# Kernel optimization log

Hardware: AMD Instinct MI355X
Metric: run time of the kernel (lower is better)

Reference implementation:

```python
import jax, jax.numpy as jnp
import numpy as np
from jax import lax


def setup_inputs() -> dict:
    key = jax.random.key(0)
    ks = jax.random.split(key, 14)
    B, T, I, H = 64, 512, 1024, 1024
    s = 0.02  # small init so gates stay in a sane range
    inp = {"x": jax.random.normal(ks[0], (B, T, I), jnp.float32)}
    names = ["wii", "whi", "bi", "wif", "whf", "bf", "wig", "whg", "bg", "wio", "who", "bo"]
    shapes = [(I, H), (H, H), (H,)] * 4
    for n, sh, k in zip(names, shapes, ks[1:]):
        inp[n] = jax.random.normal(k, sh, jnp.float32) * s
    return inp


def reference(x, wii, whi, bi, wif, whf, bf, wig, whg, bg, wio, who, bo):
    B, T, _ = x.shape
    H = bi.shape[0]
    # Pack the 4 gates (i, f, g, o) into single GEMMs.
    Wx = jnp.concatenate([wii, wif, wig, wio], axis=1)  # [I, 4H]
    Wh = jnp.concatenate([whi, whf, whg, who], axis=1)  # [H, 4H]
    b = jnp.concatenate([bi, bf, bg, bo])               # [4H]
    # Precompute all input projections in one big GEMM: [B, T, 4H]
    xproj = jnp.einsum("bti,ig->btg", x, Wx) + b

    def step(carry, xt):
        ht, ct = carry  # [B, H] each
        gates = xt + ht @ Wh  # [B, 4H]
        i = jax.nn.sigmoid(gates[:, 0 * H:1 * H])
        f = jax.nn.sigmoid(gates[:, 1 * H:2 * H])
        g = jnp.tanh(gates[:, 2 * H:3 * H])
        o = jax.nn.sigmoid(gates[:, 3 * H:4 * H])
        ct = f * ct + i * g
        ht = o * jnp.tanh(ct)
        return (ht, ct), ht

    h0 = jnp.zeros((B, H), x.dtype)
    c0 = jnp.zeros((B, H), x.dtype)
    (ht, ct), hseq = lax.scan(step, (h0, c0), xproj.transpose(1, 0, 2))
    hseq = hseq.transpose(1, 0, 2)  # [B, T, H]
    return hseq, ht, ct
```

## Files before the change

### kernel.cpp

```cpp
#include <hip/hip_runtime.h>
#include <cstddef>
#include <cstdint>


typedef __bf16 bf16_t;
typedef __bf16 bf16x8 __attribute__((ext_vector_type(8)));
typedef __bf16 bf16x4 __attribute__((ext_vector_type(4)));
typedef float  f32x4  __attribute__((ext_vector_type(4)));

#define MFMA16(a, b, c) __builtin_amdgcn_mfma_f32_16x16x32_bf16((a), (b), (c), 0, 0, 0)

#define BB   64
#define TT   512
#define HH   1024
#define G4H  4096

#define XPROJ_OFF  0ull
#define WX_OFF     268435456ull
#define WH_OFF     (WX_OFF + 8388608ull)
#define BC_OFF     (WH_OFF + 8388608ull)
#define HB_OFF     (BC_OFF + 16384ull)
#define BAR_OFF    (HB_OFF + 262144ull)

__device__ __forceinline__ float fsig(float x) {
    return 1.0f / (1.0f + __expf(-x));
}
__device__ __forceinline__ float ftanh(float x) {
    return 1.0f - 2.0f / (__expf(2.0f * x) + 1.0f);
}

__global__ void transpose_pack(const float* __restrict__ s0, const float* __restrict__ s1,
                               const float* __restrict__ s2, const float* __restrict__ s3,
                               const float* __restrict__ s4, const float* __restrict__ s5,
                               const float* __restrict__ s6, const float* __restrict__ s7,
                               bf16_t* __restrict__ wxt, bf16_t* __restrict__ wht) {
    __shared__ float tile[64][65];
    const int z = blockIdx.z;
    const float* src = (z == 0) ? s0 : (z == 1) ? s1 : (z == 2) ? s2 : (z == 3) ? s3
                      : (z == 4) ? s4 : (z == 5) ? s5 : (z == 6) ? s6 : s7;
    bf16_t* dst = ((z < 4) ? wxt : wht) + (size_t)(z & 3) * 1024 * 1024;
    const int k0 = blockIdx.x * 64, h0 = blockIdx.y * 64;
    const int t = threadIdx.x;
#pragma unroll
    for (int i = 0; i < 16; ++i) {
        int kk = (t >> 6) * 16 + i, hh = t & 63;
        tile[kk][hh] = src[(size_t)(k0 + kk) * 1024 + h0 + hh];
    }
    __syncthreads();
#pragma unroll
    for (int i = 0; i < 16; ++i) {
        int hh = (t >> 6) * 16 + i, kk = t & 63;
        dst[(size_t)(h0 + hh) * 1024 + k0 + kk] = (bf16_t)tile[kk][hh];
    }
}

__global__ void pack_bias(const float* __restrict__ bi, const float* __restrict__ bf_,
                          const float* __restrict__ bg, const float* __restrict__ bo,
                          float* __restrict__ bc) {
    int n = blockIdx.x * 256 + threadIdx.x;
    int g = n >> 10, h = n & 1023;
    const float* s = (g == 0) ? bi : (g == 1) ? bf_ : (g == 2) ? bg : bo;
    bc[n] = s[h];
}

__global__ __launch_bounds__(256, 2) void gemm_xproj(
    const float* __restrict__ x, const bf16_t* __restrict__ wx,
    const float* __restrict__ bc, bf16_t* __restrict__ xp) {
    __shared__ bf16_t Als[128][72];
    __shared__ bf16_t Bls[128][72];
    const int tid = threadIdx.x;
    const int n0 = blockIdx.x * 128, m0 = blockIdx.y * 128;
    const int lane = tid & 63, w = tid >> 6;
    const int wm = w >> 1, wn = w & 1;
    const int col = lane & 15, quad = lane >> 4;
    const int rowA = tid >> 4, ksegA = (tid & 15) * 4;
    const int rowB = tid >> 3, chunkB = tid & 7;
    f32x4 acc[4][4] = {};

    for (int kt = 0; kt < 16; ++kt) {
        const int k0 = kt * 64;
        __syncthreads();
#pragma unroll
        for (int i = 0; i < 8; ++i) {
            int r = rowA + i * 16;
            float4 v = *(const float4*)&x[(size_t)(m0 + r) * 1024 + k0 + ksegA];
            bf16x4 pv = { (bf16_t)v.x, (bf16_t)v.y, (bf16_t)v.z, (bf16_t)v.w };
            *(bf16x4*)&Als[r][ksegA] = pv;
        }
#pragma unroll
        for (int i = 0; i < 4; ++i) {
            int r = rowB + i * 32;
            *(bf16x8*)&Bls[r][chunkB * 8] =
                *(const bf16x8*)&wx[(size_t)(n0 + r) * 1024 + k0 + chunkB * 8];
        }
        __syncthreads();
#pragma unroll
        for (int kq = 0; kq < 64; kq += 32) {
            bf16x8 a[4], b[4];
#pragma unroll
            for (int s = 0; s < 4; ++s) {
                a[s] = *(const bf16x8*)&Als[wm * 64 + s * 16 + col][kq + quad * 8];
                b[s] = *(const bf16x8*)&Bls[wn * 64 + s * 16 + col][kq + quad * 8];
            }
#pragma unroll
            for (int sm = 0; sm < 4; ++sm)
#pragma unroll
                for (int sn = 0; sn < 4; ++sn)
                    acc[sm][sn] = MFMA16(a[sm], b[sn], acc[sm][sn]);
        }
    }
#pragma unroll
    for (int sm = 0; sm < 4; ++sm) {
        int mbase = m0 + wm * 64 + sm * 16 + quad * 4;
#pragma unroll
        for (int sn = 0; sn < 4; ++sn) {
            int n = n0 + wn * 64 + sn * 16 + col;
            float bias = bc[n];
#pragma unroll
            for (int reg = 0; reg < 4; ++reg) {
                int mm = mbase + reg;
                int b = mm >> 9, t = mm & 511;
                xp[(size_t)((t << 6) + b) * 4096 + n] = (bf16_t)(acc[sm][sn][reg] + bias);
            }
        }
    }
}

__global__ __launch_bounds__(256, 1) void lstm_rec(
    const bf16_t* __restrict__ xproj, const bf16_t* __restrict__ whc,
    bf16_t* __restrict__ hbuf, float* __restrict__ out,
    unsigned int* __restrict__ bar) {
    __shared__ bf16_t wh[16][1032];
    __shared__ float  gl[64][17];
    __shared__ __align__(8) unsigned short gl2[64][4];
    const int tid = threadIdx.x;
    const int bid = blockIdx.x;
    unsigned int* goflag = bar + 384;

    {
        int r = tid >> 4, sub = tid & 15;
        int n = (r >> 2) * 1024 + bid * 4 + (r & 3);
        const bf16_t* src = whc + (size_t)n * 1024;
#pragma unroll
        for (int j = 0; j < 8; ++j) {
            int e = (j * 16 + sub) * 8;
            *(bf16x8*)&wh[r][e] = *(const bf16x8*)&src[e];
        }
    }
    __syncthreads();

    const int w = tid >> 6, lane = tid & 63;
    const int col = lane & 15, quad = lane >> 4;
    const int rowA = w * 16 + col;
    const int bb0  = w * 16 + quad * 4;
    const int b2 = tid >> 2, cc = tid & 3;
    const int hcol = bid * 4 + cc;
    const int ng = (col >> 2) * 1024 + bid * 4 + (col & 3);

    float cstate = 0.0f;
    float* hseq = out;
    float* hT = out + (size_t)BB * TT * HH;
    float* cT = hT + BB * HH;

    float xpre[4];
#pragma unroll
    for (int reg = 0; reg < 4; ++reg)
        xpre[reg] = (float)xproj[(size_t)(bb0 + reg) * 4096 + ng];

    for (int t = 0; t < TT; ++t) {
        const bf16_t* hprev = hbuf + (size_t)(t & 1) * (BB * HH);
        bf16_t* hnext = hbuf + (size_t)((t + 1) & 1) * (BB * HH);

        const bf16_t* hbase = hprev + (size_t)rowA * 1024 + quad * 8;
        bf16x8 af[32];
#define LDH(i, o) asm volatile("global_load_dwordx4 %0, %1, off offset:" o " sc0 sc1" \
                               : "=v"(af[i]) : "v"(hbase))
        LDH(0, "0");     LDH(1, "64");    LDH(2, "128");   LDH(3, "192");
        LDH(4, "256");   LDH(5, "320");   LDH(6, "384");   LDH(7, "448");
        LDH(8, "512");   LDH(9, "576");   LDH(10, "640");  LDH(11, "704");
        LDH(12, "768");  LDH(13, "832");  LDH(14, "896");  LDH(15, "960");
        LDH(16, "1024"); LDH(17, "1088"); LDH(18, "1152"); LDH(19, "1216");
        LDH(20, "1280"); LDH(21, "1344"); LDH(22, "1408"); LDH(23, "1472");
        LDH(24, "1536"); LDH(25, "1600"); LDH(26, "1664"); LDH(27, "1728");
        LDH(28, "1792"); LDH(29, "1856"); LDH(30, "1920"); LDH(31, "1984");
#undef LDH
        asm volatile("s_waitcnt vmcnt(0)" ::: "memory");
        __builtin_amdgcn_sched_barrier(0);

        f32x4 acc = {0.f, 0.f, 0.f, 0.f};
#pragma unroll
        for (int kq = 0; kq < 32; ++kq) {
            bf16x8 bfr = *(const bf16x8*)&wh[col][kq * 32 + quad * 8];
            acc = MFMA16(af[kq], bfr, acc);
        }

#pragma unroll
        for (int reg = 0; reg < 4; ++reg) {
            int bb = bb0 + reg;
            gl[bb][col] = acc[reg] + xpre[reg];
        }

        float iv = fsig(gl[b2][cc]);
        float fv = fsig(gl[b2][4 + cc]);
        float gv = ftanh(gl[b2][8 + cc]);
        float ov = fsig(gl[b2][12 + cc]);
        cstate = fv * cstate + iv * gv;
        float hv = ov * ftanh(cstate);

        __builtin_nontemporal_store(hv, &hseq[(size_t)b2 * (TT * HH) + t * HH + hcol]);
        bf16_t hvb = (bf16_t)hv;
        gl2[b2][cc] = *(const unsigned short*)&hvb;

        if (t == TT - 1) {
            __builtin_nontemporal_store(hv, &hT[b2 * HH + hcol]);
            __builtin_nontemporal_store(cstate, &cT[b2 * HH + hcol]);
            break;
        }

        __syncthreads();

        const unsigned tgt = (unsigned)(t + 1);
        const size_t xoff = (size_t)((t + 1) * 64 + bb0) * 4096 + ng;
        if (w == 0) {
            unsigned long long pk = *(const unsigned long long*)&gl2[lane][0];
            __hip_atomic_store((unsigned long long*)(hnext + (size_t)lane * HH + bid * 4),
                               pk, __ATOMIC_RELAXED, __HIP_MEMORY_SCOPE_AGENT);
            asm volatile("s_waitcnt vmcnt(0)" ::: "memory");
            if (lane == 0)
                __hip_atomic_store(&bar[bid], tgt, __ATOMIC_RELAXED,
                                   __HIP_MEMORY_SCOPE_AGENT);
            asm volatile("" ::: "memory");
#pragma unroll
            for (int reg = 0; reg < 4; ++reg)
                xpre[reg] = (float)xproj[xoff + (size_t)reg * 4096];

            if (bid == 0) {
                unsigned int* sl = bar + lane * 4;
                for (;;) {
                    unsigned v0 = __hip_atomic_load(sl + 0, __ATOMIC_RELAXED,
                                                    __HIP_MEMORY_SCOPE_AGENT);
                    unsigned v1 = __hip_atomic_load(sl + 1, __ATOMIC_RELAXED,
                                                    __HIP_MEMORY_SCOPE_AGENT);
                    unsigned v2 = __hip_atomic_load(sl + 2, __ATOMIC_RELAXED,
                                                    __HIP_MEMORY_SCOPE_AGENT);
                    unsigned v3 = __hip_atomic_load(sl + 3, __ATOMIC_RELAXED,
                                                    __HIP_MEMORY_SCOPE_AGENT);
                    int ok = (v0 >= tgt) & (v1 >= tgt) & (v2 >= tgt) & (v3 >= tgt);
                    if (__all(ok)) break;
                    __builtin_amdgcn_s_sleep(2);
                }
                if (lane == 0)
                    __hip_atomic_store(goflag, tgt, __ATOMIC_RELAXED,
                                       __HIP_MEMORY_SCOPE_AGENT);
            } else {
                for (;;) {
                    unsigned g = __hip_atomic_load(goflag, __ATOMIC_RELAXED,
                                                   __HIP_MEMORY_SCOPE_AGENT);
                    if (g >= tgt) break;
                    __builtin_amdgcn_s_sleep(2);
                }
            }
        } else {
#pragma unroll
            for (int reg = 0; reg < 4; ++reg)
                xpre[reg] = (float)xproj[xoff + (size_t)reg * 4096];
        }
        __syncthreads();
    }
}

extern "C" void kernel_launch(void* const* d_in, const int* in_sizes, int n_in,
                              void* d_out, int out_size, void* d_ws, size_t ws_size,
                              hipStream_t stream) {
    (void)in_sizes; (void)n_in; (void)out_size; (void)ws_size;
    const float* x   = (const float*)d_in[0];
    const float* wii = (const float*)d_in[1];
    const float* whi = (const float*)d_in[2];
    const float* bi  = (const float*)d_in[3];
    const float* wif = (const float*)d_in[4];
    const float* whf = (const float*)d_in[5];
    const float* bfb = (const float*)d_in[6];
    const float* wig = (const float*)d_in[7];
    const float* whg = (const float*)d_in[8];
    const float* bg  = (const float*)d_in[9];
    const float* wio = (const float*)d_in[10];
    const float* who = (const float*)d_in[11];
    const float* bo  = (const float*)d_in[12];

    char* ws = (char*)d_ws;
    bf16_t*   xp   = (bf16_t*)(ws + XPROJ_OFF);
    bf16_t*   wxt  = (bf16_t*)(ws + WX_OFF);
    bf16_t*   wht  = (bf16_t*)(ws + WH_OFF);
    float*    bc   = (float*)(ws + BC_OFF);
    bf16_t*   hbuf = (bf16_t*)(ws + HB_OFF);
    unsigned* bar  = (unsigned*)(ws + BAR_OFF);

    hipMemsetAsync(hbuf, 0, 262144 + 4096, stream);

    transpose_pack<<<dim3(16, 16, 8), 256, 0, stream>>>(wii, wif, wig, wio,
                                                        whi, whf, whg, who, wxt, wht);
    pack_bias<<<16, 256, 0, stream>>>(bi, bfb, bg, bo, bc);
    gemm_xproj<<<dim3(32, 256), 256, 0, stream>>>(x, wxt, bc, xp);
    lstm_rec<<<256, 256, 0, stream>>>(xp, wht, hbuf, (float*)d_out, bar);
}
```

Baseline: 4.723 ms.

## Halve recurrent grid to 128 blocks with 8 hidden columns each and flat barrier

Each persistent block of the recurrent kernel now owns 8 hidden units (32 gate rows) instead of 4, so the grid drops from 256 to 128 blocks, each issuing two MFMA chains over the same loaded h fragment. The two-level barrier (block 0 gathers, then broadcasts a go flag) becomes a flat barrier where every block polls all 128 flags directly. Each thread now handles two adjacent units with packed bf16 xproj loads and writes h to the global buffer itself. The aim is to halve redundant h reads, cut the barrier's serial hop and shrink per-step latency, at the cost of more per-block MFMA work and more polling traffic.

```diff
diff --git a/kernel.cpp b/kernel.cpp
--- a/kernel.cpp
+++ b/kernel.cpp
@@ -6,7 +6,9 @@
 typedef __bf16 bf16_t;
 typedef __bf16 bf16x8 __attribute__((ext_vector_type(8)));
 typedef __bf16 bf16x4 __attribute__((ext_vector_type(4)));
+typedef __bf16 bf16x2 __attribute__((ext_vector_type(2)));
 typedef float  f32x4  __attribute__((ext_vector_type(4)));
+typedef float  f32x2  __attribute__((ext_vector_type(2)));
 
 #define MFMA16(a, b, c) __builtin_amdgcn_mfma_f32_16x16x32_bf16((a), (b), (c), 0, 0, 0)
 
@@ -14,6 +16,7 @@
 #define TT   512
 #define HH   1024
 #define G4H  4096
+#define NBLK 128
 
 #define XPROJ_OFF  0ull
 #define WX_OFF     268435456ull
@@ -130,20 +133,17 @@
     const bf16_t* __restrict__ xproj, const bf16_t* __restrict__ whc,
     bf16_t* __restrict__ hbuf, float* __restrict__ out,
     unsigned int* __restrict__ bar) {
-    __shared__ bf16_t wh[16][1032];
-    __shared__ float  gl[64][17];
-    __shared__ __align__(8) unsigned short gl2[64][4];
+    __shared__ bf16_t wh[32][1032];
+    __shared__ float  gl[64][36];
     const int tid = threadIdx.x;
     const int bid = blockIdx.x;
-    unsigned int* goflag = bar + 384;
 
     {
-        int r = tid >> 4, sub = tid & 15;
-        int n = (r >> 2) * 1024 + bid * 4 + (r & 3);
-        const bf16_t* src = whc + (size_t)n * 1024;
-#pragma unroll
-        for (int j = 0; j < 8; ++j) {
-            int e = (j * 16 + sub) * 8;
+        int r = tid >> 3, seg = tid & 7;
+        const bf16_t* src = whc + (size_t)((r >> 3) * 1024 + bid * 8 + (r & 7)) * 1024;
+#pragma unroll
+        for (int j = 0; j < 16; ++j) {
+            int e = seg * 128 + j * 8;
             *(bf16x8*)&wh[r][e] = *(const bf16x8*)&src[e];
         }
     }
@@ -153,19 +153,19 @@
     const int col = lane & 15, quad = lane >> 4;
     const int rowA = w * 16 + col;
     const int bb0  = w * 16 + quad * 4;
-    const int b2 = tid >> 2, cc = tid & 3;
-    const int hcol = bid * 4 + cc;
-    const int ng = (col >> 2) * 1024 + bid * 4 + (col & 3);
-
-    float cstate = 0.0f;
+    const int b2 = tid >> 2;
+    const int c2 = (tid & 3) * 2;
+    const int hcol = bid * 8 + c2;
+
+    float cs0 = 0.0f, cs1 = 0.0f;
     float* hseq = out;
     float* hT = out + (size_t)BB * TT * HH;
     float* cT = hT + BB * HH;
 
-    float xpre[4];
-#pragma unroll
-    for (int reg = 0; reg < 4; ++reg)
-        xpre[reg] = (float)xproj[(size_t)(bb0 + reg) * 4096 + ng];
+    unsigned xq[4];
+#pragma unroll
+    for (int g = 0; g < 4; ++g)
+        xq[g] = *(const unsigned*)&xproj[(size_t)b2 * 4096 + g * 1024 + hcol];
 
     for (int t = 0; t < TT; ++t) {
         const bf16_t* hprev = hbuf + (size_t)(t & 1) * (BB * HH);
@@ -187,83 +187,75 @@
         asm volatile("s_waitcnt vmcnt(0)" ::: "memory");
         __builtin_amdgcn_sched_barrier(0);
 
-        f32x4 acc = {0.f, 0.f, 0.f, 0.f};
+        f32x4 acc0 = {0.f, 0.f, 0.f, 0.f};
+        f32x4 acc1 = {0.f, 0.f, 0.f, 0.f};
 #pragma unroll
         for (int kq = 0; kq < 32; ++kq) {
-            bf16x8 bfr = *(const bf16x8*)&wh[col][kq * 32 + quad * 8];
-            acc = MFMA16(af[kq], bfr, acc);
+            bf16x8 b0 = *(const bf16x8*)&wh[col][kq * 32 + quad * 8];
+            bf16x8 b1 = *(const bf16x8*)&wh[16 + col][kq * 32 + quad * 8];
+            acc0 = MFMA16(af[kq], b0, acc0);
+            acc1 = MFMA16(af[kq], b1, acc1);
         }
 
 #pragma unroll
         for (int reg = 0; reg < 4; ++reg) {
-            int bb = bb0 + reg;
-            gl[bb][col] = acc[reg] + xpre[reg];
-        }
-
-        float iv = fsig(gl[b2][cc]);
-        float fv = fsig(gl[b2][4 + cc]);
-        float gv = ftanh(gl[b2][8 + cc]);
-        float ov = fsig(gl[b2][12 + cc]);
-        cstate = fv * cstate + iv * gv;
-        float hv = ov * ftanh(cstate);
-
-        __builtin_nontemporal_store(hv, &hseq[(size_t)b2 * (TT * HH) + t * HH + hcol]);
-        bf16_t hvb = (bf16_t)hv;
-        gl2[b2][cc] = *(const unsigned short*)&hvb;
+            gl[bb0 + reg][col]      = acc0[reg];
+            gl[bb0 + reg][16 + col] = acc1[reg];
+        }
+
+        float a0l = gl[b2][0 * 8 + c2]     + __uint_as_float(xq[0] << 16);
+        float a0h = gl[b2][0 * 8 + c2 + 1] + __uint_as_float(xq[0] & 0xffff0000u);
+        float a1l = gl[b2][1 * 8 + c2]     + __uint_as_float(xq[1] << 16);
+        float a1h = gl[b2][1 * 8 + c2 + 1] + __uint_as_float(xq[1] & 0xffff0000u);
+        float a2l = gl[b2][2 * 8 + c2]     + __uint_as_float(xq[2] << 16);
+        float a2h = gl[b2][2 * 8 + c2 + 1] + __uint_as_float(xq[2] & 0xffff0000u);
+        float a3l = gl[b2][3 * 8 + c2]     + __uint_as_float(xq[3] << 16);
+        float a3h = gl[b2][3 * 8 + c2 + 1] + __uint_as_float(xq[3] & 0xffff0000u);
+        cs0 = fsig(a1l) * cs0 + fsig(a0l) * ftanh(a2l);
+        cs1 = fsig(a1h) * cs1 + fsig(a0h) * ftanh(a2h);
+        float hv0 = fsig(a3l) * ftanh(cs0);
+        float hv1 = fsig(a3h) * ftanh(cs1);
+
+        f32x2 hv2 = { hv0, hv1 };
+        __builtin_nontemporal_store(hv2, (f32x2*)&hseq[(size_t)b2 * (TT * HH) + t * HH + hcol]);
+
+        bf16x2 hb2 = { (bf16_t)hv0, (bf16_t)hv1 };
+        unsigned hpk = __builtin_bit_cast(unsigned, hb2);
+        __hip_atomic_store((unsigned*)(hnext + (size_t)b2 * HH + hcol), hpk,
+                           __ATOMIC_RELAXED, __HIP_MEMORY_SCOPE_AGENT);
 
         if (t == TT - 1) {
-            __builtin_nontemporal_store(hv, &hT[b2 * HH + hcol]);
-            __builtin_nontemporal_store(cstate, &cT[b2 * HH + hcol]);
+            __builtin_nontemporal_store(hv2, (f32x2*)&hT[(size_t)b2 * HH + hcol]);
+            f32x2 cv2 = { cs0, cs1 };
+            __builtin_nontemporal_store(cv2, (f32x2*)&cT[(size_t)b2 * HH + hcol]);
             break;
         }
 
         __syncthreads();
 
         const unsigned tgt = (unsigned)(t + 1);
-        const size_t xoff = (size_t)((t + 1) * 64 + bb0) * 4096 + ng;
+        const size_t xoff = (size_t)((t + 1) * 64 + b2) * 4096 + bid * 8 + c2;
         if (w == 0) {
-            unsigned long long pk = *(const unsigned long long*)&gl2[lane][0];
-            __hip_atomic_store((unsigned long long*)(hnext + (size_t)lane * HH + bid * 4),
-                               pk, __ATOMIC_RELAXED, __HIP_MEMORY_SCOPE_AGENT);
             asm volatile("s_waitcnt vmcnt(0)" ::: "memory");
             if (lane == 0)
                 __hip_atomic_store(&bar[bid], tgt, __ATOMIC_RELAXED,
                                    __HIP_MEMORY_SCOPE_AGENT);
             asm volatile("" ::: "memory");
 #pragma unroll
-            for (int reg = 0; reg < 4; ++reg)
-                xpre[reg] = (float)xproj[xoff + (size_t)reg * 4096];
-
-            if (bid == 0) {
-                unsigned int* sl = bar + lane * 4;
-                for (;;) {
-                    unsigned v0 = __hip_atomic_load(sl + 0, __ATOMIC_RELAXED,
-                                                    __HIP_MEMORY_SCOPE_AGENT);
-                    unsigned v1 = __hip_atomic_load(sl + 1, __ATOMIC_RELAXED,
-                                                    __HIP_MEMORY_SCOPE_AGENT);
-                    unsigned v2 = __hip_atomic_load(sl + 2, __ATOMIC_RELAXED,
-                                                    __HIP_MEMORY_SCOPE_AGENT);
-                    unsigned v3 = __hip_atomic_load(sl + 3, __ATOMIC_RELAXED,
-                                                    __HIP_MEMORY_SCOPE_AGENT);
-                    int ok = (v0 >= tgt) & (v1 >= tgt) & (v2 >= tgt) & (v3 >= tgt);
-                    if (__all(ok)) break;
-                    __builtin_amdgcn_s_sleep(2);
-                }
-                if (lane == 0)
-                    __hip_atomic_store(goflag, tgt, __ATOMIC_RELAXED,
-                                       __HIP_MEMORY_SCOPE_AGENT);
-            } else {
-                for (;;) {
-                    unsigned g = __hip_atomic_load(goflag, __ATOMIC_RELAXED,
-                                                   __HIP_MEMORY_SCOPE_AGENT);
-                    if (g >= tgt) break;
-                    __builtin_amdgcn_s_sleep(2);
-                }
+            for (int g = 0; g < 4; ++g)
+                xq[g] = *(const unsigned*)&xproj[xoff + (size_t)g * 1024];
+            for (;;) {
+                unsigned v0 = __hip_atomic_load(bar + lane, __ATOMIC_RELAXED,
+                                                __HIP_MEMORY_SCOPE_AGENT);
+                unsigned v1 = __hip_atomic_load(bar + 64 + lane, __ATOMIC_RELAXED,
+                                                __HIP_MEMORY_SCOPE_AGENT);
+                if (__all((v0 >= tgt) & (v1 >= tgt))) break;
+                __builtin_amdgcn_s_sleep(1);
             }
         } else {
 #pragma unroll
-            for (int reg = 0; reg < 4; ++reg)
-                xpre[reg] = (float)xproj[xoff + (size_t)reg * 4096];
+            for (int g = 0; g < 4; ++g)
+                xq[g] = *(const unsigned*)&xproj[xoff + (size_t)g * 1024];
         }
         __syncthreads();
     }
@@ -295,11 +287,11 @@
     bf16_t*   hbuf = (bf16_t*)(ws + HB_OFF);
     unsigned* bar  = (unsigned*)(ws + BAR_OFF);
 
-    hipMemsetAsync(hbuf, 0, 262144 + 4096, stream);
+    (void)hipMemsetAsync(hbuf, 0, 262144 + 4096, stream);
 
     transpose_pack<<<dim3(16, 16, 8), 256, 0, stream>>>(wii, wif, wig, wio,
                                                         whi, whf, whg, who, wxt, wht);
     pack_bias<<<16, 256, 0, stream>>>(bi, bfb, bg, bo, bc);
     gemm_xproj<<<dim3(32, 256), 256, 0, stream>>>(x, wxt, bc, xp);
-    lstm_rec<<<256, 256, 0, stream>>>(xp, wht, hbuf, (float*)d_out, bar);
-}
+    lstm_rec<<<NBLK, 256, 0, stream>>>(xp, wht, hbuf, (float*)d_out, bar);
+}
```

Result: slower. 5.071 ms (+7.4%).
